# Kernel optimization log

Measured on AMD Instinct MI355X. Metric: run time of the kernel, lower is better.

The kernel has to match this reference:

```python
import jax, jax.numpy as jnp
import numpy as np
from jax import lax

PAD = 40
MAX_DISP = 40
STRIDE2 = 1
CORR_MULT = 1.0


def _correlation1d(input1, input2):
    # input1, input2: [B, C, H, W]; kernel_size=1, stride1=1
    B, C, H, W = input1.shape
    D = 2 * MAX_DISP // STRIDE2 + 1  # 81 displacement channels
    # zero-pad input2 along the width dimension
    in2p = jnp.pad(input2, ((0, 0), (0, 0), (0, 0), (PAD, PAD)))
    offsets = jnp.arange(D, dtype=jnp.int32) * STRIDE2  # start col in padded map; disp = off - PAD

    def body(carry, off):
        shifted = lax.dynamic_slice(in2p, (0, 0, 0, off), (B, C, H, W))
        # mean over channels (sumelems = kernel_size^2 * C = C)
        c = jnp.sum(input1 * shifted, axis=1) / C  # [B, H, W]
        return carry, c

    _, corr = lax.scan(body, None, offsets)  # [D, B, H, W]
    out = jnp.transpose(corr, (1, 0, 2, 3)) * CORR_MULT  # [B, D, H, W]
    return out


def setup_inputs() -> dict:
    key = jax.random.key(0)
    k1, k2 = jax.random.split(key)
    input1 = jax.random.normal(k1, (8, 256, 96, 192), dtype=jnp.float32)
    input2 = jax.random.normal(k2, (8, 256, 96, 192), dtype=jnp.float32)
    return {"input1": input1, "input2": input2}


def reference(input1, input2):
    return _correlation1d(input1, input2)
```

## Files before the change

### kernel.cpp

```cpp
#include <hip/hip_runtime.h>


typedef __attribute__((ext_vector_type(8))) short short8;
typedef __attribute__((ext_vector_type(4))) float float4v;
typedef __attribute__((ext_vector_type(4))) int int4v;

__device__ __forceinline__ unsigned short f2bf(float f) {
  unsigned int u = __float_as_uint(f);
  return (unsigned short)((u + 0x7FFFu + ((u >> 16) & 1u)) >> 16);
}

__global__ __launch_bounds__(64, 3) void corr1d_kernel(
    const float* __restrict__ in1, const float* __restrict__ in2,
    float* __restrict__ out) {
  constexpr int W = 192, H = 96, C = 256, D = 81;
  constexpr int HW = H * W;
  constexpr int KC = 32;
  constexpr int SB = 40;
  constexpr int WCH = 48;

  __shared__ __align__(16) unsigned short smem[128 * SB];
  unsigned short* B_l = smem;
  float* E = (float*)smem;

  const int bx = blockIdx.x;
  const int q  = bx & 3;
  const int bh = bx >> 2;
  const int b = bh / H;
  const int h = bh % H;
  const int lane = threadIdx.x;
  const int l15 = lane & 15;
  const int lq  = lane >> 4;

  const int w0abs = WCH * q;
  const int lo = (w0abs - 40 > 0) ? (w0abs - 40) : 0;
  const int hi = (w0abs + 88 < W) ? (w0abs + 88) : W;
  const int nbg = (hi - lo) >> 2;
  const int jr0 = lo + 40 - w0abs;

  if (q == 0) {
    for (int t = lane; t < 160; t += 64) {
      int j = t >> 2, kg = t & 3;
      *(int4v*)(B_l + j * SB + kg * 8) = (int4v){0, 0, 0, 0};
    }
  } else if (q == 3) {
    for (int t = lane; t < 160; t += 64) {
      int j = 88 + (t >> 2), kg = t & 3;
      *(int4v*)(B_l + j * SB + kg * 8) = (int4v){0, 0, 0, 0};
    }
  }

  float4v acc[3][6];
#pragma unroll
  for (int i = 0; i < 3; ++i)
#pragma unroll
    for (int jj = 0; jj < 6; ++jj) acc[i][jj] = (float4v){0.f, 0.f, 0.f, 0.f};

  const int base = (b * C * H + h) * W;
  const float* a_col = in1 + base + w0abs + l15;
  const int ntasks = nbg * 4;

  for (int c0 = 0; c0 < C; c0 += KC) {
    float a_raw[3][8];
#pragma unroll
    for (int i = 0; i < 3; ++i)
#pragma unroll
      for (int t = 0; t < 8; ++t)
        a_raw[i][t] = a_col[(c0 + 8 * lq + t) * HW + 16 * i];

    for (int t = lane; t < ntasks; t += 64) {
      const int cg = t & 3;
      const int wg = t >> 2;
      const int gaddr = base + (c0 + cg * 8) * HW + lo + 4 * wg;
      float4v v[8];
#pragma unroll
      for (int i = 0; i < 8; ++i) v[i] = *(const float4v*)(in2 + gaddr + i * HW);
      const int jr = jr0 + 4 * wg;
#pragma unroll
      for (int x = 0; x < 4; ++x) {
        unsigned short o[8];
#pragma unroll
        for (int i = 0; i < 8; ++i) o[i] = f2bf(v[i][x]);
        *(int4v*)(B_l + (jr + x) * SB + cg * 8) = *(const int4v*)o;
      }
    }

    short8 af[3];
#pragma unroll
    for (int i = 0; i < 3; ++i) {
      unsigned short o[8];
#pragma unroll
      for (int t = 0; t < 8; ++t) o[t] = f2bf(a_raw[i][t]);
      af[i] = *(const short8*)o;
    }

#pragma unroll
    for (int jt = 0; jt < 8; ++jt) {
      short8 bfr = *(const short8*)(B_l + (16 * jt + l15) * SB + 8 * lq);
#pragma unroll
      for (int i = 0; i < 3; ++i) {
        const int jj = jt - i;
        if (jj >= 0 && jj < 6)
          acc[i][jj] = __builtin_amdgcn_mfma_f32_16x16x32_bf16(
              af[i], bfr, acc[i][jj], 0, 0, 0);
      }
    }
  }

  const float scale = 1.0f / 256.0f;
#pragma unroll
  for (int p = 0; p < 2; ++p) {
    const int dlo = p ? 41 : 0;
    const int nd  = p ? 40 : 41;
#pragma unroll
    for (int i = 0; i < 3; ++i)
#pragma unroll
      for (int jj = 0; jj < 6; ++jj)
#pragma unroll
        for (int r = 0; r < 4; ++r) {
          const int d  = 16 * jj + l15 - 4 * lq - r;
          const int wr = 16 * i + 4 * lq + r;
          if (d >= dlo && d < dlo + nd)
            E[(d - dlo) * 48 + wr] = acc[i][jj][r] * scale;
        }
    for (int t = lane; t < nd * 12; t += 64) {
      const int dr = t / 12, g = t % 12;
      float4v val = *(const float4v*)(E + dr * 48 + 4 * g);
      *(float4v*)(out + ((b * D + dlo + dr) * H + h) * W + w0abs + 4 * g) = val;
    }
  }
}

extern "C" void kernel_launch(void* const* d_in, const int* in_sizes, int n_in,
                              void* d_out, int out_size, void* d_ws, size_t ws_size,
                              hipStream_t stream) {
  const float* in1 = (const float*)d_in[0];
  const float* in2 = (const float*)d_in[1];
  float* out = (float*)d_out;
  (void)in_sizes; (void)n_in; (void)out_size; (void)d_ws; (void)ws_size;
  corr1d_kernel<<<dim3(3072), dim3(64), 0, stream>>>(in1, in2, out);
}
```

Before: 344.9 us.

## Software-pipeline global loads of A and B across channel chunks

```diff
diff --git a/kernel.cpp b/kernel.cpp
--- a/kernel.cpp
+++ b/kernel.cpp
@@ -15,9 +15,7 @@
     float* __restrict__ out) {
   constexpr int W = 192, H = 96, C = 256, D = 81;
   constexpr int HW = H * W;
-  constexpr int KC = 32;
   constexpr int SB = 40;
-  constexpr int WCH = 48;
 
   __shared__ __align__(16) unsigned short smem[128 * SB];
   unsigned short* B_l = smem;
@@ -32,7 +30,7 @@
   const int l15 = lane & 15;
   const int lq  = lane >> 4;
 
-  const int w0abs = WCH * q;
+  const int w0abs = 48 * q;
   const int lo = (w0abs - 40 > 0) ? (w0abs - 40) : 0;
   const int hi = (w0abs + 88 < W) ? (w0abs + 88) : W;
   const int nbg = (hi - lo) >> 2;
@@ -40,13 +38,13 @@
 
   if (q == 0) {
     for (int t = lane; t < 160; t += 64) {
-      int j = t >> 2, kg = t & 3;
-      *(int4v*)(B_l + j * SB + kg * 8) = (int4v){0, 0, 0, 0};
+      int j = t >> 2, g = t & 3;
+      *(int4v*)(B_l + j * SB + 8 * g) = (int4v){0, 0, 0, 0};
     }
   } else if (q == 3) {
     for (int t = lane; t < 160; t += 64) {
-      int j = 88 + (t >> 2), kg = t & 3;
-      *(int4v*)(B_l + j * SB + kg * 8) = (int4v){0, 0, 0, 0};
+      int j = 88 + (t >> 2), g = t & 3;
+      *(int4v*)(B_l + j * SB + 8 * g) = (int4v){0, 0, 0, 0};
     }
   }
 
@@ -58,33 +56,49 @@
 
   const int base = (b * C * H + h) * W;
   const float* a_col = in1 + base + w0abs + l15;
-  const int ntasks = nbg * 4;
 
-  for (int c0 = 0; c0 < C; c0 += KC) {
-    float a_raw[3][8];
+  const bool bact = lane < 2 * nbg;
+  const int bcg = lane & 1;
+  const int bwg = lane >> 1;
+  const float* bsrc = in2 + base + lo + 4 * bwg;
+  const int brow0 = jr0 + 4 * bwg;
+
+  float4v bv[8];
+  float a_raw[3][8];
+
+  auto burstB = [&](int c0, int h2) {
+    if (bact) {
+      const float* p = bsrc + (c0 + 16 * h2 + 8 * bcg) * HW;
 #pragma unroll
-    for (int i = 0; i < 3; ++i)
-#pragma unroll
-      for (int t = 0; t < 8; ++t)
-        a_raw[i][t] = a_col[(c0 + 8 * lq + t) * HW + 16 * i];
-
-    for (int t = lane; t < ntasks; t += 64) {
-      const int cg = t & 3;
-      const int wg = t >> 2;
-      const int gaddr = base + (c0 + cg * 8) * HW + lo + 4 * wg;
-      float4v v[8];
-#pragma unroll
-      for (int i = 0; i < 8; ++i) v[i] = *(const float4v*)(in2 + gaddr + i * HW);
-      const int jr = jr0 + 4 * wg;
+      for (int i = 0; i < 8; ++i) bv[i] = *(const float4v*)(p + i * HW);
+    }
+  };
+  auto stageB = [&](int h2) {
+    if (bact) {
+      const int ko = 16 * h2 + 8 * bcg;
 #pragma unroll
       for (int x = 0; x < 4; ++x) {
         unsigned short o[8];
 #pragma unroll
-        for (int i = 0; i < 8; ++i) o[i] = f2bf(v[i][x]);
-        *(int4v*)(B_l + (jr + x) * SB + cg * 8) = *(const int4v*)o;
+        for (int i = 0; i < 8; ++i) o[i] = f2bf(bv[i][x]);
+        *(int4v*)(B_l + (brow0 + x) * SB + ko) = *(const int4v*)o;
       }
     }
+  };
+  auto burstA = [&](int c0) {
+#pragma unroll
+    for (int i2 = 0; i2 < 3; ++i2)
+#pragma unroll
+      for (int t = 0; t < 8; ++t)
+        a_raw[i2][t] = a_col[(c0 + 8 * lq + t) * HW + 16 * i2];
+  };
 
+  burstA(0);
+  burstB(0, 0);
+
+  for (int c0 = 0; c0 < C; c0 += 32) {
+    stageB(0);
+    burstB(c0, 1);
     short8 af[3];
 #pragma unroll
     for (int i = 0; i < 3; ++i) {
@@ -93,7 +107,11 @@
       for (int t = 0; t < 8; ++t) o[t] = f2bf(a_raw[i][t]);
       af[i] = *(const short8*)o;
     }
-
+    stageB(1);
+    if (c0 + 32 < C) {
+      burstA(c0 + 32);
+      burstB(c0 + 32, 0);
+    }
 #pragma unroll
     for (int jt = 0; jt < 8; ++jt) {
       short8 bfr = *(const short8*)(B_l + (16 * jt + l15) * SB + 8 * lq);
```

Measured after the change: 342.8 us. About the same (-0.6%).
